# Kernel tuning notes

Hardware: AMD Instinct MI355X
Metric: run time of the kernel (lower is better)

The kernel has to match this reference:

```python
import jax, jax.numpy as jnp
import numpy as np

V, B, NP, NJ = 5, 32, 20, 17
NB = 16
ND = 128
POSE_MIN_DEPTH, POSE_MAX_DEPTH = 2000.0, 8000.0
POSE_SIGMA = 100.0
KS = 11
HIDDEN_ROUGH, HIDDEN = 1024, 1024
BONES = np.array([[0,1],[0,2],[1,3],[2,4],[5,6],[5,7],[7,9],[6,8],[8,10],[5,11],[6,12],[11,12],[11,13],[13,15],[12,14],[14,16]], dtype=np.int32)


def setup_inputs() -> dict:
    key = jax.random.key(0)
    ks = jax.random.split(key, 12)
    wh = jnp.array([1920.0, 1080.0], jnp.float32)
    kpts = jax.random.uniform(ks[0], (V, B, NP, NJ, 2), jnp.float32) * wh
    pose_vis = jnp.ones((V, B, NP), jnp.float32)
    joint_vis = (jax.random.uniform(ks[1], (V, B, NP, NJ)) > 0.15).astype(jnp.float32)
    gt_pose_depths = jax.random.uniform(ks[2], (B, NP), jnp.float32, 2000.0, 8000.0)
    gt_joint_depths = jax.random.uniform(ks[3], (B, NP, NJ), jnp.float32, -100.0, 100.0)
    angles = np.linspace(-0.3, 0.3, V)
    Rs = np.stack([np.array([[np.cos(a), 0.0, np.sin(a)], [0.0, 1.0, 0.0], [-np.sin(a), 0.0, np.cos(a)]], dtype=np.float32) for a in angles])
    cam_R = jnp.broadcast_to(jnp.asarray(Rs)[:, None], (V, B, 3, 3))
    tvec = np.zeros((V, 3), np.float32); tvec[:, 0] = np.linspace(-500.0, 500.0, V)
    cam_T = jnp.broadcast_to(jnp.asarray(tvec)[:, None], (V, B, 3))
    cam_f = jnp.full((V, B, 2), 1400.0, jnp.float32)
    cam_c = jnp.broadcast_to(jnp.array([960.0, 540.0], jnp.float32), (V, B, 2))
    image_wh = jnp.broadcast_to(jnp.array([1920.0, 1080.0], jnp.float32), (V, B, 2))
    num_persons = jax.random.randint(ks[4], (V, B), 10, NP + 1, jnp.int32)
    Wr1 = jax.random.normal(ks[5], (HIDDEN_ROUGH, NJ * 2)) * 0.02
    br1 = jnp.zeros((HIDDEN_ROUGH,), jnp.float32)
    Wr2 = jax.random.normal(ks[6], (NJ, HIDDEN_ROUGH)) * 0.02
    br2 = jnp.zeros((NJ,), jnp.float32)
    Wc1 = jax.random.normal(ks[7], (HIDDEN, NJ + NB, 3)) * 0.02
    bc1 = jnp.zeros((HIDDEN,), jnp.float32)
    Wc2 = jax.random.normal(ks[8], (1, HIDDEN, 3)) * 0.02
    bc2 = jnp.zeros((1,), jnp.float32)
    bones = jnp.asarray(BONES)
    return dict(kpts=kpts, pose_vis=pose_vis, joint_vis=joint_vis, gt_pose_depths=gt_pose_depths, gt_joint_depths=gt_joint_depths, cam_R=cam_R, cam_T=cam_T, cam_f=cam_f, cam_c=cam_c, image_wh=image_wh, num_persons=num_persons, Wr1=Wr1, br1=br1, Wr2=Wr2, br2=br2, Wc1=Wc1, bc1=bc1, Wc2=Wc2, bc2=bc2, bones=bones)


def _bone_len(p, bones):
    # p: [B, Np, Nj, D, 2] -> [B, Np, Nb, D]
    a = p[:, :, bones[:, 0]]
    b = p[:, :, bones[:, 1]]
    return jnp.sqrt(jnp.sum((a - b) ** 2, -1) + 1e-12)


def _conv1d(x, w, b):
    # x [N,C,L], w [O,I,3]
    y = jax.lax.conv_general_dilated(x, w, (1,), 'SAME', dimension_numbers=('NCH', 'OIH', 'NCH'))
    return y + b[None, :, None]


def _forward(kpts, joint_vis, cam_R, cam_T, cam_f, cam_c, image_wh, num_persons, Wr1, br1, Wr2, br2, Wc1, bc1, Wc2, bc2, bones):
    V_, B_, NP_, NJ_, _ = kpts.shape
    labels = jnp.arange(ND, dtype=jnp.float32) / (ND - 1) * (POSE_MAX_DEPTH - POSE_MIN_DEPTH) + POSE_MIN_DEPTH
    kt = kpts[0]  # target-view 2D poses [B,Np,Nj,2]
    # faithful to original indexing quirk: normalize all batches by batch-0 image size
    kn = kt / image_wh[0, 0][None, None, None, :]
    x = kn.reshape(B_ * NP_, NJ_ * 2)
    h = jax.nn.relu(x @ Wr1.T + br1)
    rough = (h @ Wr2.T + br2).reshape(B_, NP_, NJ_) * 1000.0
    rough = jax.lax.stop_gradient(rough)  # .detach() in original
    depths = labels[None, None, None, :] + rough[..., None]  # [B,Np,Nj,D]
    # back-project target 2D poses at every depth hypothesis
    R0, T0, f0, c0 = cam_R[0], cam_T[0], cam_f[0], cam_c[0]
    uvn = (kt - c0[:, None, None, :]) / f0[:, None, None, :]
    xy = uvn[..., None, :] * depths[..., None]
    cam_pts = jnp.concatenate([xy, depths[..., None]], -1)
    p3d = jnp.einsum('bji,bpkdj->bpkdi', R0, cam_pts) + T0[:, None, None, None, :]  # world [B,Np,Nj,D,3]

    scores = scores2 = boundings = boundings2 = None
    for rv in range(1, V_):
        Rr, Tr, fr, cr = cam_R[rv], cam_T[rv], cam_f[rv], cam_c[rv]
        xc = jnp.einsum('bij,bpkdj->bpkdi', Rr, p3d - Tr[:, None, None, None, :])
        p2t = xc[..., :2] / (xc[..., 2:3] + 1e-8) * fr[:, None, None, None, :] + cr[:, None, None, None, :]
        pr = kpts[rv]         # [B,Npr,Nj,2]
        vr = joint_vis[rv]    # [B,Npr,Nj]
        # pairwise dist over (target-person, ref-person) per joint/depth
        d = jnp.sum((p2t[:, :, None] - pr[:, None, :, :, None, :]) ** 2, -1)  # [B,Npt,Npr,Nj,D]
        w = vr[:, None, :, :, None]
        pdist = jnp.sum(d * w, 3) / (jnp.sum(w, 3) + 1e-8)  # [B,Npt,Npr,D]
        valid = jnp.arange(NP_)[None, None, :, None] < num_persons[rv][:, None, None, None]
        pdist = jnp.where(valid, pdist, 1e5)
        mm = jnp.argmin(pdist, 2)  # [B,Npt,D] nearest ref pose
        bidx = jnp.arange(B_)[:, None, None]
        matched = jnp.transpose(pr[bidx, mm], (0, 1, 3, 2, 4))  # [B,Npt,Nj,D,2]
        mvis = jnp.transpose(vr[bidx, mm], (0, 1, 3, 2))        # [B,Npt,Nj,D]
        mdist = jnp.sum((p2t - matched) ** 2, -1)
        score = jnp.exp(-jnp.sqrt(mdist + 1e-12) / POSE_SIGMA)  # panoptic branch
        score_bl = jnp.exp(-jnp.abs(_bone_len(matched, bones) - _bone_len(p2t, bones)) / 5.0)
        wimg = image_wh[rv][:, None, None, None, 0]
        himg = image_wh[rv][:, None, None, None, 1]
        inb = ((p2t[..., 0] >= 0) & (p2t[..., 1] >= 0) & (p2t[..., 0] <= wimg - 1) & (p2t[..., 1] <= himg - 1)).astype(score.dtype)
        bounding = inb * mvis
        bounding2 = jnp.broadcast_to(mvis[:, :, :1, :], score_bl.shape)
        if scores is None:
            scores, scores2 = score * bounding, score_bl * bounding2
            boundings, boundings2 = bounding, bounding2
        else:
            scores = scores + score * bounding
            scores2 = scores2 + score_bl * bounding2
            boundings = boundings + bounding
            boundings2 = boundings2 + bounding2
    psv = (scores / (boundings + 1e-8)).reshape(B_ * NP_, NJ_, ND)
    psv2 = (scores2 / (boundings2 + 1e-8)).reshape(B_ * NP_, NB, ND)
    xin = jnp.concatenate([psv, psv2], 1)  # [BN, Nj+Nb, D]
    hc = jax.nn.relu(_conv1d(xin, Wc1, bc1))
    logits = _conv1d(hc, Wc2, bc2)[:, 0, :]  # [BN, D]
    vol = jax.nn.softmax(logits, -1)
    # soft-argmax restricted to a window around the argmax
    pos = jnp.arange(ND, dtype=vol.dtype)
    idx = jnp.argmax(vol, -1)
    mask = (jnp.abs(pos[None, :] - idx[:, None].astype(vol.dtype)) <= KS // 2).astype(vol.dtype)
    mv = vol * mask
    mv = mv / (jnp.sum(mv, -1, keepdims=True) + 1e-8)
    pred_idx = jnp.sum(mv * pos, -1).reshape(B_, NP_)
    return pred_idx / (ND - 1) * (POSE_MAX_DEPTH - POSE_MIN_DEPTH) + POSE_MIN_DEPTH


def reference(kpts, pose_vis, joint_vis, gt_pose_depths, gt_joint_depths, cam_R, cam_T, cam_f, cam_c, image_wh, num_persons, Wr1, br1, Wr2, br2, Wc1, bc1, Wc2, bc2, bones):
    return _forward(kpts, joint_vis, cam_R, cam_T, cam_f, cam_c, image_wh, num_persons, Wr1, br1, Wr2, br2, Wc1, bc1, Wc2, bc2, bones)
```

## Files before the change

kernel.cpp:

```cpp
#include <hip/hip_runtime.h>
#include <math.h>

#define VV  5
#define BB  32
#define NPP 20
#define NJJ 17
#define NBB 16
#define NDD 128
#define HID 1024
#define KPITCH 128
#define KSTEPS 7
#define PRP 36
#define VRP 20
#define NCH 34
#define A_T_ELEMS (32 * KSTEPS * 64 * 8)
#define EPI_ELEMS (32 * 4 * 64 * 16)

typedef __attribute__((ext_vector_type(8))) short short8;
typedef __attribute__((ext_vector_type(16))) float float16;

static constexpr int BONE_A[NBB] = {0,0,1,2,5,5,7,6,8,5,6,11,11,13,12,14};
static constexpr int BONE_B[NBB] = {1,2,3,4,6,7,9,8,10,11,12,12,13,15,14,16};

__device__ __forceinline__ float warp_red_sum(float v) {
#pragma unroll
  for (int off = 32; off >= 1; off >>= 1) v += __shfl_xor(v, off, 64);
  return v;
}

__global__ __launch_bounds__(256) void prep_kernel(
    const float* __restrict__ Wc1, const float* __restrict__ Wc2,
    const float* __restrict__ bc1,
    unsigned short* __restrict__ A_hi, unsigned short* __restrict__ A_lo,
    float* __restrict__ epi) {
  int gidx = blockIdx.x * 256 + threadIdx.x;
  if (gidx < A_T_ELEMS) {
    int e = gidx & 7;
    int l = (gidx >> 3) & 63;
    int rest = gidx >> 9;
    int ks = rest % 7;
    int ot = rest / 7;
    int o = ot * 32 + (l & 31);
    int kk = ks * 16 + (l >> 5) * 8 + e;
    float x = (kk < 99) ? Wc1[o * 99 + kk] : 0.0f;
    unsigned int u = __float_as_uint(x);
    unsigned short hi = (unsigned short)(u >> 16);
    float xh = __uint_as_float((u >> 16) << 16);
    unsigned short lo = (unsigned short)(__float_as_uint(x - xh) >> 16);
    A_hi[gidx] = hi;
    A_lo[gidx] = lo;
  } else {
    int idx2 = gidx - A_T_ELEMS;
    if (idx2 < EPI_ELEMS) {
      int c = idx2 & 15;
      int l = (idx2 >> 4) & 63;
      int rb = (idx2 >> 10) & 3;
      int ot = idx2 >> 12;
      int base = ot * 32 + 4 * (l >> 5) + 8 * rb;
      epi[idx2] = (c < 12) ? Wc2[base * 3 + c] : bc1[base + (c - 12)];
    }
  }
}

__global__ __launch_bounds__(512, 4) void pose_front_kernel(
    const float* __restrict__ kpts, const float* __restrict__ joint_vis,
    const float* __restrict__ cam_R, const float* __restrict__ cam_T,
    const float* __restrict__ cam_f, const float* __restrict__ cam_c,
    const float* __restrict__ image_wh, const int* __restrict__ num_persons,
    const float* __restrict__ Wr1, const float* __restrict__ br1,
    const float* __restrict__ Wr2, const float* __restrict__ br2,
    float* __restrict__ ws_partial) {
  const int n = blockIdx.x;
  const int b = n / NPP;
  const int p = n % NPP;
  const int tid = threadIdx.x;
  const int wv = tid >> 6, ln = tid & 63;
  const int rvv = tid >> 7;
  const int d   = tid & (NDD - 1);

  __shared__ float sh_x[NJJ * 2];
  __shared__ float sh_h[HID];
  __shared__ float sh_rough[NJJ];
  __shared__ float sh_base[NJJ][3];
  __shared__ __align__(16) float sh_pr[4][NPP][PRP];
  __shared__ __align__(16) float sh_vr[4][NPP][VRP];

  if (tid < NJJ * 2) {
    int j = tid >> 1, c = tid & 1;
    float k = kpts[((size_t)(b * NPP + p)) * NJJ * 2 + j * 2 + c];
    sh_x[tid] = k / image_wh[c];
  }
  __syncthreads();

#pragma unroll
  for (int k = 0; k < 2; ++k) {
    int m = tid + k * 512;
    float acc = br1[m];
#pragma unroll
    for (int c = 0; c < NJJ * 2; ++c) acc = fmaf(Wr1[m * (NJJ * 2) + c], sh_x[c], acc);
    sh_h[m] = fmaxf(acc, 0.0f);
  }
  __syncthreads();

  for (int j = wv; j < NJJ; j += 8) {
    float part = 0.0f;
    for (int m = ln; m < HID; m += 64) part = fmaf(Wr2[j * HID + m], sh_h[m], part);
    part = warp_red_sum(part);
    if (ln == 0) sh_rough[j] = (part + br2[j]) * 1000.0f;
  }
  if (tid < NJJ) {
    int j = tid;
    const float* R0 = cam_R + (size_t)b * 9;
    float c0x = cam_c[b * 2 + 0], c0y = cam_c[b * 2 + 1];
    float f0x = cam_f[b * 2 + 0], f0y = cam_f[b * 2 + 1];
    float kx = kpts[((size_t)(b * NPP + p)) * NJJ * 2 + j * 2 + 0];
    float ky = kpts[((size_t)(b * NPP + p)) * NJJ * 2 + j * 2 + 1];
    float ux = (kx - c0x) / f0x;
    float uy = (ky - c0y) / f0y;
#pragma unroll
    for (int i = 0; i < 3; ++i)
      sh_base[j][i] = R0[0 * 3 + i] * ux + R0[1 * 3 + i] * uy + R0[2 * 3 + i];
  }
#pragma unroll
  for (int rr = 0; rr < 4; ++rr) {
    const float* prg = kpts + ((size_t)(rr + 1) * BB + b) * NPP * NJJ * 2;
    for (int idx = tid; idx < NPP * NJJ * 2; idx += 512)
      sh_pr[rr][idx / 34][idx % 34] = prg[idx];
    const float* vrg = joint_vis + ((size_t)(rr + 1) * BB + b) * NPP * NJJ;
    for (int idx = tid; idx < NPP * NJJ; idx += 512)
      sh_vr[rr][idx / 17][idx % 17] = vrg[idx];
  }
  if (tid < 4 * BB) {
    int rr = tid >> 5, q = tid & 31;
    if (q < NPP) {
      sh_pr[rr][q][34] = 0.0f; sh_pr[rr][q][35] = 0.0f;
      sh_vr[rr][q][17] = 0.0f; sh_vr[rr][q][18] = 0.0f; sh_vr[rr][q][19] = 0.0f;
    }
  }
  __syncthreads();

  {
    const int rv = rvv + 1;
    const int vb = rv * BB + b;
    const float* Rr = cam_R + (size_t)vb * 9;
    const float R00 = Rr[0], R01 = Rr[1], R02 = Rr[2];
    const float R10 = Rr[3], R11 = Rr[4], R12 = Rr[5];
    const float R20 = Rr[6], R21 = Rr[7], R22 = Rr[8];
    const float Trx = cam_T[vb * 3 + 0], Try = cam_T[vb * 3 + 1], Trz = cam_T[vb * 3 + 2];
    const float frx = cam_f[vb * 2 + 0], fry = cam_f[vb * 2 + 1];
    const float crx = cam_c[vb * 2 + 0], cry = cam_c[vb * 2 + 1];
    const float wmax = image_wh[vb * 2 + 0] - 1.0f;
    const float hmax = image_wh[vb * 2 + 1] - 1.0f;
    const int nprv = num_persons[vb];
    const float T0x = cam_T[b * 3 + 0], T0y = cam_T[b * 3 + 1], T0z = cam_T[b * 3 + 2];
    const float lab = ((float)d / 127.0f) * 6000.0f + 2000.0f;

    float px[NJJ], py[NJJ];
#pragma unroll
    for (int j = 0; j < NJJ; ++j) {
      float dep = lab + sh_rough[j];
      float p0 = fmaf(dep, sh_base[j][0], T0x);
      float p1 = fmaf(dep, sh_base[j][1], T0y);
      float p2 = fmaf(dep, sh_base[j][2], T0z);
      float q0 = p0 - Trx, q1 = p1 - Try, q2 = p2 - Trz;
      float xc0 = R00 * q0 + R01 * q1 + R02 * q2;
      float xc1 = R10 * q0 + R11 * q1 + R12 * q2;
      float xc2 = R20 * q0 + R21 * q1 + R22 * q2 + 1e-8f;
      px[j] = xc0 / xc2 * frx + crx;
      py[j] = xc1 / xc2 * fry + cry;
    }

    float best = 3.4e38f;
    int mm = 0;
#pragma unroll 1
    for (int q = 0; q < NPP; ++q) {
      const float4* pr4 = (const float4*)(&sh_pr[rvv][q][0]);
      const float4* vr4 = (const float4*)(&sh_vr[rvv][q][0]);
      float num = 0.0f, den = 0.0f;
#pragma unroll
      for (int g4 = 0; g4 < 4; ++g4) {
        float4 w  = vr4[g4];
        float4 pa = pr4[2 * g4 + 0];
        float4 pb = pr4[2 * g4 + 1];
        { float dx = px[4*g4+0] - pa.x, dy = py[4*g4+0] - pa.y; num = fmaf(w.x, dx*dx + dy*dy, num); den += w.x; }
        { float dx = px[4*g4+1] - pa.z, dy = py[4*g4+1] - pa.w; num = fmaf(w.y, dx*dx + dy*dy, num); den += w.y; }
        { float dx = px[4*g4+2] - pb.x, dy = py[4*g4+2] - pb.y; num = fmaf(w.z, dx*dx + dy*dy, num); den += w.z; }
        { float dx = px[4*g4+3] - pb.z, dy = py[4*g4+3] - pb.w; num = fmaf(w.w, dx*dx + dy*dy, num); den += w.w; }
      }
      {
        float w16 = sh_vr[rvv][q][16];
        float4 pc = pr4[8];
        float dx = px[16] - pc.x, dy = py[16] - pc.y;
        num = fmaf(w16, dx*dx + dy*dy, num); den += w16;
      }
      float pd = num / (den + 1e-8f);
      if (q >= nprv) pd = 100000.0f;
      if (pd < best) { best = pd; mm = q; }
    }

    float* pbase = ws_partial + (((size_t)n * NCH) * 4 + rvv) * 128 + d;
    unsigned int maskB = 0u;
#pragma unroll
    for (int j = 0; j < NJJ; ++j) {
      float mx = sh_pr[rvv][mm][j * 2 + 0];
      float my = sh_pr[rvv][mm][j * 2 + 1];
      float mv = sh_vr[rvv][mm][j];
      float dx = px[j] - mx, dy = py[j] - my;
      float sc = expf(-sqrtf(dx * dx + dy * dy + 1e-12f) / 100.0f);
      float inb = (px[j] >= 0.0f && py[j] >= 0.0f && px[j] <= wmax && py[j] <= hmax) ? 1.0f : 0.0f;
      float bd = inb * mv;
      pbase[j * 512] = sc * bd;
      maskB |= ((unsigned int)(bd != 0.0f)) << j;
    }
    float v0 = sh_vr[rvv][mm][0];
    maskB |= ((unsigned int)(v0 != 0.0f)) << 17;
#pragma unroll
    for (int nb = 0; nb < NBB; ++nb) {
      const int a = BONE_A[nb], c = BONE_B[nb];
      float ax = sh_pr[rvv][mm][a * 2 + 0], ay = sh_pr[rvv][mm][a * 2 + 1];
      float cx = sh_pr[rvv][mm][c * 2 + 0], cy = sh_pr[rvv][mm][c * 2 + 1];
      float dmx = ax - cx, dmy = ay - cy;
      float blm = sqrtf(dmx * dmx + dmy * dmy + 1e-12f);
      float dpx = px[a] - px[c], dpy = py[a] - py[c];
      float blp = sqrtf(dpx * dpx + dpy * dpy + 1e-12f);
      float scb = expf(-fabsf(blm - blp) / 5.0f);
      pbase[(NJJ + nb) * 512] = scb * v0;
    }
    *(unsigned int*)(pbase + 33 * 512) = maskB;
  }
}

__global__ __launch_bounds__(128) void reduce_kernel(
    const float* __restrict__ ws_partial, float* __restrict__ ws_xin) {
  const int n = blockIdx.x;
  const int t = threadIdx.x;
  const float* pb = ws_partial + ((size_t)n * NCH) * 4 * 128;
  float* xo = ws_xin + (size_t)n * (NJJ + NBB) * NDD;

  unsigned int m0 = __float_as_uint(pb[(33 * 4 + 0) * 128 + t]);
  unsigned int m1 = __float_as_uint(pb[(33 * 4 + 1) * 128 + t]);
  unsigned int m2 = __float_as_uint(pb[(33 * 4 + 2) * 128 + t]);
  unsigned int m3 = __float_as_uint(pb[(33 * 4 + 3) * 128 + t]);

#pragma unroll
  for (int i = 0; i < NJJ; ++i) {
    const float* a = pb + (i * 4) * 128 + t;
    float s = ((a[0] + a[128]) + a[256]) + a[384];
    int bj = ((m0 >> i) & 1) + ((m1 >> i) & 1) + ((m2 >> i) & 1) + ((m3 >> i) & 1);
    xo[i * NDD + t] = s / ((float)bj + 1e-8f);
  }
  int b2 = ((m0 >> 17) & 1) + ((m1 >> 17) & 1) + ((m2 >> 17) & 1) + ((m3 >> 17) & 1);
  float den2 = (float)b2 + 1e-8f;
#pragma unroll
  for (int nb = 0; nb < NBB; ++nb) {
    const float* a = pb + ((NJJ + nb) * 4) * 128 + t;
    float s = ((a[0] + a[128]) + a[256]) + a[384];
    xo[(NJJ + nb) * NDD + t] = s / den2;
  }
}

__global__ __launch_bounds__(512, 2) void conv_mfma_kernel(
    const float* __restrict__ ws_xin,
    const unsigned short* __restrict__ A_hi, const unsigned short* __restrict__ A_lo,
    const float* __restrict__ epi,
    const float* __restrict__ bc2, float* __restrict__ out) {
  const int n = blockIdx.x;
  const int tid = threadIdx.x;
  const int w = tid >> 6;
  const int l = tid & 63;
  const int lrow = l & 31;
  const int g = l >> 5;

  __shared__ __align__(16) unsigned short bT_hi[128 * KPITCH];
  __shared__ __align__(16) unsigned short bT_lo[128 * KPITCH];
  __shared__ float plg[3][8][NDD];
  __shared__ float sh_l[NDD];
  __shared__ float sh_e[NDD];
  __shared__ float sh_sc[2];

  for (int i = tid; i < 3 * 8 * NDD; i += 512) ((float*)plg)[i] = 0.0f;

  const float* xn = ws_xin + (size_t)n * (NJJ + NBB) * NDD;
  for (int idx = tid; idx < 64 * 128; idx += 512) {
    const int kp = (idx & 63) << 1;
    const int t  = idx >> 6;
    unsigned int hp = 0, lp = 0;
#pragma unroll
    for (int u = 0; u < 2; ++u) {
      const int kk = kp + u;
      float x = 0.0f;
      if (kk < 99) {
        int i3 = kk / 3;
        int k3 = kk - i3 * 3;
        int tt = t + k3 - 1;
        if (tt >= 0 && tt < 128) x = xn[i3 * NDD + tt];
      }
      unsigned int uu = __float_as_uint(x);
      unsigned int hi = uu >> 16;
      float xh = __uint_as_float(hi << 16);
      unsigned int lo = __float_as_uint(x - xh) >> 16;
      hp |= hi << (16 * u);
      lp |= lo << (16 * u);
    }
    const int e = t * KPITCH + (kp ^ ((t & 15) << 3));
    *(unsigned int*)(bT_hi + e) = hp;
    *(unsigned int*)(bT_lo + e) = lp;
  }
  __syncthreads();

#pragma unroll 1
  for (int otile = 0; otile < 4; ++otile) {
    const int otg = w * 4 + otile;

    short8 Ah[KSTEPS], Al[KSTEPS];
    {
      const short8* ahT = ((const short8*)A_hi) + (size_t)otg * KSTEPS * 64 + l;
      const short8* alT = ((const short8*)A_lo) + (size_t)otg * KSTEPS * 64 + l;
#pragma unroll
      for (int ks = 0; ks < KSTEPS; ++ks) {
        Ah[ks] = ahT[ks * 64];
        Al[ks] = alT[ks * 64];
      }
    }
    float w2f[48];
    float bcf[16];
#pragma unroll
    for (int rb = 0; rb < 4; ++rb) {
      const float4* ep = ((const float4*)epi) + ((size_t)(otg * 4 + rb) * 64 + l) * 4;
      float4 e0 = ep[0], e1 = ep[1], e2 = ep[2], e3 = ep[3];
      w2f[rb * 12 + 0] = e0.x;  w2f[rb * 12 + 1] = e0.y;  w2f[rb * 12 + 2] = e0.z;
      w2f[rb * 12 + 3] = e0.w;  w2f[rb * 12 + 4] = e1.x;  w2f[rb * 12 + 5] = e1.y;
      w2f[rb * 12 + 6] = e1.z;  w2f[rb * 12 + 7] = e1.w;  w2f[rb * 12 + 8] = e2.x;
      w2f[rb * 12 + 9] = e2.y;  w2f[rb * 12 + 10] = e2.z; w2f[rb * 12 + 11] = e2.w;
      bcf[rb * 4 + 0] = e3.x; bcf[rb * 4 + 1] = e3.y;
      bcf[rb * 4 + 2] = e3.z; bcf[rb * 4 + 3] = e3.w;
    }

#pragma unroll 1
    for (int ttile = 0; ttile < 4; ++ttile) {
      const int trow = ttile * 32 + lrow;
      const unsigned short* brh = bT_hi + trow * KPITCH;
      const unsigned short* brl = bT_lo + trow * KPITCH;
      const int sw = (trow & 15) << 3;

      float16 X, Y;
#pragma unroll
      for (int r = 0; r < 16; ++r) { X[r] = 0.0f; Y[r] = 0.0f; }

#pragma unroll
      for (int ks = 0; ks < KSTEPS; ++ks) {
        const int e = (ks * 16 + g * 8) ^ sw;
        short8 bh = *(const short8*)(brh + e);
        X = __builtin_amdgcn_mfma_f32_32x32x16_bf16(Ah[ks], bh, X, 0, 0, 0);
        Y = __builtin_amdgcn_mfma_f32_32x32x16_bf16(Al[ks], bh, Y, 0, 0, 0);
      }
#pragma unroll
      for (int ks = 0; ks < KSTEPS; ++ks) {
        const int e = (ks * 16 + g * 8) ^ sw;
        short8 bl = *(const short8*)(brl + e);
        if (ks & 1) Y = __builtin_amdgcn_mfma_f32_32x32x16_bf16(Ah[ks], bl, Y, 0, 0, 0);
        else        X = __builtin_amdgcn_mfma_f32_32x32x16_bf16(Ah[ks], bl, X, 0, 0, 0);
      }

      float sP = 0.0f, sC = 0.0f, sM = 0.0f;
#pragma unroll
      for (int r = 0; r < 16; ++r) {
        float h = fmaxf((X[r] + Y[r]) + bcf[(r >> 2) * 4 + (r & 3)], 0.0f);
        sP = fmaf(h, w2f[(r >> 2) * 12 + (r & 3) * 3 + 0], sP);
        sC = fmaf(h, w2f[(r >> 2) * 12 + (r & 3) * 3 + 1], sC);
        sM = fmaf(h, w2f[(r >> 2) * 12 + (r & 3) * 3 + 2], sM);
      }
      sP += __shfl_xor(sP, 32, 64);
      sC += __shfl_xor(sC, 32, 64);
      sM += __shfl_xor(sM, 32, 64);
      if (l < 32) {
        plg[0][w][trow] += sP;
        plg[1][w][trow] += sC;
        plg[2][w][trow] += sM;
      }
    }
  }
  __syncthreads();

  if (tid < NDD) {
    int t = tid;
    float lg = bc2[0];
#pragma unroll
    for (int ww = 0; ww < 8; ++ww) lg += plg[1][ww][t];
    if (t > 0) {
#pragma unroll
      for (int ww = 0; ww < 8; ++ww) lg += plg[0][ww][t - 1];
    }
    if (t < NDD - 1) {
#pragma unroll
      for (int ww = 0; ww < 8; ++ww) lg += plg[2][ww][t + 1];
    }
    sh_l[t] = lg;
  }
  __syncthreads();
  if (tid < 64) {
    float v1 = sh_l[tid], v2 = sh_l[tid + 64];
    float mv; int mi;
    if (v2 > v1) { mv = v2; mi = tid + 64; } else { mv = v1; mi = tid; }
#pragma unroll
    for (int off = 32; off >= 1; off >>= 1) {
      float ov = __shfl_xor(mv, off, 64);
      int   oi = __shfl_xor(mi, off, 64);
      if (ov > mv || (ov == mv && oi < mi)) { mv = ov; mi = oi; }
    }
    if (tid == 0) { sh_sc[0] = mv; ((int*)sh_sc)[1] = mi; }
  }
  __syncthreads();
  const float gmax = sh_sc[0];
  const int gidx = ((const int*)sh_sc)[1];
  if (tid < NDD) sh_e[tid] = expf(sh_l[tid] - gmax);
  __syncthreads();
  if (tid < 64) {
    float S = warp_red_sum(sh_e[tid] + sh_e[tid + 64]);
    float a1 = 0.0f, a2 = 0.0f;
#pragma unroll
    for (int k = 0; k < 2; ++k) {
      int t = tid + k * 64;
      float vol = sh_e[t] / S;
      float msk = (fabsf((float)t - (float)gidx) <= 5.0f) ? 1.0f : 0.0f;
      float mvv = vol * msk;
      a1 += mvv;
      a2 += mvv * (float)t;
    }
    a1 = warp_red_sum(a1);
    a2 = warp_red_sum(a2);
    if (tid == 0) {
      float pred = a2 / (a1 + 1e-8f);
      out[n] = pred / 127.0f * 6000.0f + 2000.0f;
    }
  }
}

extern "C" void kernel_launch(void* const* d_in, const int* in_sizes, int n_in,
                              void* d_out, int out_size, void* d_ws, size_t ws_size,
                              hipStream_t stream) {
  (void)in_sizes; (void)n_in; (void)out_size; (void)ws_size;
  const float* kpts        = (const float*)d_in[0];
  const float* joint_vis   = (const float*)d_in[2];
  const float* cam_R       = (const float*)d_in[5];
  const float* cam_T       = (const float*)d_in[6];
  const float* cam_f       = (const float*)d_in[7];
  const float* cam_c       = (const float*)d_in[8];
  const float* image_wh    = (const float*)d_in[9];
  const int*   num_persons = (const int*)d_in[10];
  const float* Wr1 = (const float*)d_in[11];
  const float* br1 = (const float*)d_in[12];
  const float* Wr2 = (const float*)d_in[13];
  const float* br2 = (const float*)d_in[14];
  const float* Wc1 = (const float*)d_in[15];
  const float* bc1 = (const float*)d_in[16];
  const float* Wc2 = (const float*)d_in[17];
  const float* bc2 = (const float*)d_in[18];
  float* out = (float*)d_out;

  unsigned short* A_hi = (unsigned short*)d_ws;
  unsigned short* A_lo = A_hi + A_T_ELEMS;
  float* epi        = (float*)(A_lo + A_T_ELEMS);
  float* ws_xin     = epi + EPI_ELEMS;
  float* ws_partial = ws_xin + (size_t)BB * NPP * (NJJ + NBB) * NDD;

  const int prep_items = A_T_ELEMS + EPI_ELEMS;
  hipLaunchKernelGGL(prep_kernel, dim3((prep_items + 255) / 256), dim3(256), 0, stream,
                     Wc1, Wc2, bc1, A_hi, A_lo, epi);
  hipLaunchKernelGGL(pose_front_kernel, dim3(BB * NPP), dim3(512), 0, stream,
                     kpts, joint_vis, cam_R, cam_T, cam_f, cam_c, image_wh,
                     num_persons, Wr1, br1, Wr2, br2, ws_partial);
  hipLaunchKernelGGL(reduce_kernel, dim3(BB * NPP), dim3(128), 0, stream,
                     ws_partial, ws_xin);
  hipLaunchKernelGGL(conv_mfma_kernel, dim3(BB * NPP), dim3(512), 0, stream,
                     ws_xin, A_hi, A_lo, epi, bc2, out);
}
```

Measured before the change: 181.7 us.

## Split pose front and conv kernels into finer-grained blocks over depth halves

The front kernel is split into a per-person MLP/base kernel and a matching kernel launched with two 256-thread blocks per person, each covering half the depth bins. The conv MFMA kernel likewise runs two 256-thread blocks per person over depth halves and writes partial logits to workspace. A new readout kernel then combines the halves and does the softmax and windowed soft-argmax. This doubles block count to improve occupancy and load balance across CUs. In exchange it adds two extra launches and extra global round-trips for intermediates, and each MFMA block now reloads the A fragments for 8 output tiles per wave instead of 4.

```diff
diff --git a/kernel.cpp b/kernel.cpp
--- a/kernel.cpp
+++ b/kernel.cpp
@@ -13,6 +13,8 @@
 #define PRP 36
 #define VRP 20
 #define NCH 34
+#define RGH_P 20
+#define BASE_P 52
 #define A_T_ELEMS (32 * KSTEPS * 64 * 8)
 #define EPI_ELEMS (32 * 4 * 64 * 16)
 
@@ -62,28 +64,21 @@
   }
 }
 
-__global__ __launch_bounds__(512, 4) void pose_front_kernel(
-    const float* __restrict__ kpts, const float* __restrict__ joint_vis,
-    const float* __restrict__ cam_R, const float* __restrict__ cam_T,
+__global__ __launch_bounds__(256) void pose_pre_kernel(
+    const float* __restrict__ kpts, const float* __restrict__ cam_R,
     const float* __restrict__ cam_f, const float* __restrict__ cam_c,
-    const float* __restrict__ image_wh, const int* __restrict__ num_persons,
+    const float* __restrict__ image_wh,
     const float* __restrict__ Wr1, const float* __restrict__ br1,
     const float* __restrict__ Wr2, const float* __restrict__ br2,
-    float* __restrict__ ws_partial) {
+    float* __restrict__ ws_rough, float* __restrict__ ws_base) {
   const int n = blockIdx.x;
   const int b = n / NPP;
   const int p = n % NPP;
   const int tid = threadIdx.x;
   const int wv = tid >> 6, ln = tid & 63;
-  const int rvv = tid >> 7;
-  const int d   = tid & (NDD - 1);
 
   __shared__ float sh_x[NJJ * 2];
   __shared__ float sh_h[HID];
-  __shared__ float sh_rough[NJJ];
-  __shared__ float sh_base[NJJ][3];
-  __shared__ __align__(16) float sh_pr[4][NPP][PRP];
-  __shared__ __align__(16) float sh_vr[4][NPP][VRP];
 
   if (tid < NJJ * 2) {
     int j = tid >> 1, c = tid & 1;
@@ -93,8 +88,8 @@
   __syncthreads();
 
 #pragma unroll
-  for (int k = 0; k < 2; ++k) {
-    int m = tid + k * 512;
+  for (int k = 0; k < 4; ++k) {
+    int m = tid + k * 256;
     float acc = br1[m];
 #pragma unroll
     for (int c = 0; c < NJJ * 2; ++c) acc = fmaf(Wr1[m * (NJJ * 2) + c], sh_x[c], acc);
@@ -102,12 +97,13 @@
   }
   __syncthreads();
 
-  for (int j = wv; j < NJJ; j += 8) {
+  for (int j = wv; j < NJJ; j += 4) {
     float part = 0.0f;
     for (int m = ln; m < HID; m += 64) part = fmaf(Wr2[j * HID + m], sh_h[m], part);
     part = warp_red_sum(part);
-    if (ln == 0) sh_rough[j] = (part + br2[j]) * 1000.0f;
-  }
+    if (ln == 0) ws_rough[(size_t)n * RGH_P + j] = (part + br2[j]) * 1000.0f;
+  }
+
   if (tid < NJJ) {
     int j = tid;
     const float* R0 = cam_R + (size_t)b * 9;
@@ -119,15 +115,42 @@
     float uy = (ky - c0y) / f0y;
 #pragma unroll
     for (int i = 0; i < 3; ++i)
-      sh_base[j][i] = R0[0 * 3 + i] * ux + R0[1 * 3 + i] * uy + R0[2 * 3 + i];
-  }
+      ws_base[(size_t)n * BASE_P + j * 3 + i] =
+          R0[0 * 3 + i] * ux + R0[1 * 3 + i] * uy + R0[2 * 3 + i];
+  }
+}
+
+__global__ __launch_bounds__(256, 4) void pose_match_kernel(
+    const float* __restrict__ kpts, const float* __restrict__ joint_vis,
+    const float* __restrict__ cam_R, const float* __restrict__ cam_T,
+    const float* __restrict__ cam_f, const float* __restrict__ cam_c,
+    const float* __restrict__ image_wh, const int* __restrict__ num_persons,
+    const float* __restrict__ ws_rough, const float* __restrict__ ws_base,
+    float* __restrict__ ws_partial) {
+  const int bid = blockIdx.x;
+  const int n = bid >> 1;
+  const int bh = bid & 1;
+  const int b = n / NPP;
+  const int tid = threadIdx.x;
+  const int rvv = tid >> 6;
+  const int d = bh * 64 + (tid & 63);
+
+  __shared__ float sh_rough[NJJ];
+  __shared__ float sh_base[NJJ][3];
+  __shared__ __align__(16) float sh_pr[4][NPP][PRP];
+  __shared__ __align__(16) float sh_vr[4][NPP][VRP];
+
+  if (tid < NJJ) sh_rough[tid] = ws_rough[(size_t)n * RGH_P + tid];
+  if (tid >= 64 && tid < 64 + NJJ * 3)
+    ((float*)sh_base)[tid - 64] = ws_base[(size_t)n * BASE_P + (tid - 64)];
+
 #pragma unroll
   for (int rr = 0; rr < 4; ++rr) {
     const float* prg = kpts + ((size_t)(rr + 1) * BB + b) * NPP * NJJ * 2;
-    for (int idx = tid; idx < NPP * NJJ * 2; idx += 512)
+    for (int idx = tid; idx < NPP * NJJ * 2; idx += 256)
       sh_pr[rr][idx / 34][idx % 34] = prg[idx];
     const float* vrg = joint_vis + ((size_t)(rr + 1) * BB + b) * NPP * NJJ;
-    for (int idx = tid; idx < NPP * NJJ; idx += 512)
+    for (int idx = tid; idx < NPP * NJJ; idx += 256)
       sh_vr[rr][idx / 17][idx % 17] = vrg[idx];
   }
   if (tid < 4 * BB) {
@@ -259,31 +282,31 @@
   }
 }
 
-__global__ __launch_bounds__(512, 2) void conv_mfma_kernel(
+__global__ __launch_bounds__(256, 2) void conv_mfma_kernel(
     const float* __restrict__ ws_xin,
     const unsigned short* __restrict__ A_hi, const unsigned short* __restrict__ A_lo,
     const float* __restrict__ epi,
-    const float* __restrict__ bc2, float* __restrict__ out) {
-  const int n = blockIdx.x;
+    float* __restrict__ ws_pcm) {
+  const int bid = blockIdx.x;
+  const int n = bid >> 1;
+  const int bh = bid & 1;
   const int tid = threadIdx.x;
   const int w = tid >> 6;
   const int l = tid & 63;
   const int lrow = l & 31;
   const int g = l >> 5;
 
-  __shared__ __align__(16) unsigned short bT_hi[128 * KPITCH];
-  __shared__ __align__(16) unsigned short bT_lo[128 * KPITCH];
-  __shared__ float plg[3][8][NDD];
-  __shared__ float sh_l[NDD];
-  __shared__ float sh_e[NDD];
-  __shared__ float sh_sc[2];
-
-  for (int i = tid; i < 3 * 8 * NDD; i += 512) ((float*)plg)[i] = 0.0f;
+  __shared__ __align__(16) unsigned short bT_hi[64 * KPITCH];
+  __shared__ __align__(16) unsigned short bT_lo[64 * KPITCH];
+  __shared__ float plg[3][4][64];
+
+  for (int i = tid; i < 3 * 4 * 64; i += 256) ((float*)plg)[i] = 0.0f;
 
   const float* xn = ws_xin + (size_t)n * (NJJ + NBB) * NDD;
-  for (int idx = tid; idx < 64 * 128; idx += 512) {
+  for (int idx = tid; idx < 64 * 64; idx += 256) {
     const int kp = (idx & 63) << 1;
-    const int t  = idx >> 6;
+    const int tl = idx >> 6;
+    const int tg = bh * 64 + tl;
     unsigned int hp = 0, lp = 0;
 #pragma unroll
     for (int u = 0; u < 2; ++u) {
@@ -292,7 +315,7 @@
       if (kk < 99) {
         int i3 = kk / 3;
         int k3 = kk - i3 * 3;
-        int tt = t + k3 - 1;
+        int tt = tg + k3 - 1;
         if (tt >= 0 && tt < 128) x = xn[i3 * NDD + tt];
       }
       unsigned int uu = __float_as_uint(x);
@@ -302,15 +325,15 @@
       hp |= hi << (16 * u);
       lp |= lo << (16 * u);
     }
-    const int e = t * KPITCH + (kp ^ ((t & 15) << 3));
+    const int e = tl * KPITCH + (kp ^ ((tl & 15) << 3));
     *(unsigned int*)(bT_hi + e) = hp;
     *(unsigned int*)(bT_lo + e) = lp;
   }
   __syncthreads();
 
 #pragma unroll 1
-  for (int otile = 0; otile < 4; ++otile) {
-    const int otg = w * 4 + otile;
+  for (int oi = 0; oi < 8; ++oi) {
+    const int otg = w * 8 + oi;
 
     short8 Ah[KSTEPS], Al[KSTEPS];
     {
@@ -337,7 +360,7 @@
     }
 
 #pragma unroll 1
-    for (int ttile = 0; ttile < 4; ++ttile) {
+    for (int ttile = 0; ttile < 2; ++ttile) {
       const int trow = ttile * 32 + lrow;
       const unsigned short* brh = bT_hi + trow * KPITCH;
       const unsigned short* brl = bT_lo + trow * KPITCH;
@@ -350,16 +373,16 @@
 #pragma unroll
       for (int ks = 0; ks < KSTEPS; ++ks) {
         const int e = (ks * 16 + g * 8) ^ sw;
-        short8 bh = *(const short8*)(brh + e);
-        X = __builtin_amdgcn_mfma_f32_32x32x16_bf16(Ah[ks], bh, X, 0, 0, 0);
-        Y = __builtin_amdgcn_mfma_f32_32x32x16_bf16(Al[ks], bh, Y, 0, 0, 0);
+        short8 bh8 = *(const short8*)(brh + e);
+        X = __builtin_amdgcn_mfma_f32_32x32x16_bf16(Ah[ks], bh8, X, 0, 0, 0);
+        Y = __builtin_amdgcn_mfma_f32_32x32x16_bf16(Al[ks], bh8, Y, 0, 0, 0);
       }
 #pragma unroll
       for (int ks = 0; ks < KSTEPS; ++ks) {
         const int e = (ks * 16 + g * 8) ^ sw;
-        short8 bl = *(const short8*)(brl + e);
-        if (ks & 1) Y = __builtin_amdgcn_mfma_f32_32x32x16_bf16(Ah[ks], bl, Y, 0, 0, 0);
-        else        X = __builtin_amdgcn_mfma_f32_32x32x16_bf16(Ah[ks], bl, X, 0, 0, 0);
+        short8 bl8 = *(const short8*)(brl + e);
+        if (ks & 1) Y = __builtin_amdgcn_mfma_f32_32x32x16_bf16(Ah[ks], bl8, Y, 0, 0, 0);
+        else        X = __builtin_amdgcn_mfma_f32_32x32x16_bf16(Ah[ks], bl8, X, 0, 0, 0);
       }
 
       float sP = 0.0f, sC = 0.0f, sM = 0.0f;
@@ -382,54 +405,68 @@
   }
   __syncthreads();
 
-  if (tid < NDD) {
-    int t = tid;
-    float lg = bc2[0];
-#pragma unroll
-    for (int ww = 0; ww < 8; ++ww) lg += plg[1][ww][t];
-    if (t > 0) {
-#pragma unroll
-      for (int ww = 0; ww < 8; ++ww) lg += plg[0][ww][t - 1];
-    }
-    if (t < NDD - 1) {
-#pragma unroll
-      for (int ww = 0; ww < 8; ++ww) lg += plg[2][ww][t + 1];
-    }
-    sh_l[t] = lg;
-  }
-  __syncthreads();
-  if (tid < 64) {
-    float v1 = sh_l[tid], v2 = sh_l[tid + 64];
+  if (tid < 3 * 64) {
+    const int c = tid >> 6, tl = tid & 63;
+    float s = ((plg[c][0][tl] + plg[c][1][tl]) + plg[c][2][tl]) + plg[c][3][tl];
+    ws_pcm[(((size_t)n * 2 + bh) * 3 + c) * 64 + tl] = s;
+  }
+}
+
+__global__ __launch_bounds__(128) void readout_kernel(
+    const float* __restrict__ ws_pcm, const float* __restrict__ bc2,
+    float* __restrict__ out) {
+  const int n = blockIdx.x;
+  const int t = threadIdx.x;
+
+  __shared__ float sh_l[NDD];
+  __shared__ float sh_e[NDD];
+  __shared__ float sh_sc[2];
+
+  const float* pc = ws_pcm + (size_t)n * 2 * 3 * 64;
+  float lg = bc2[0] + pc[((t >> 6) * 3 + 1) * 64 + (t & 63)];
+  if (t > 0) {
+    int tp = t - 1;
+    lg += pc[((tp >> 6) * 3 + 0) * 64 + (tp & 63)];
+  }
+  if (t < NDD - 1) {
+    int tn = t + 1;
+    lg += pc[((tn >> 6) * 3 + 2) * 64 + (tn & 63)];
+  }
+  sh_l[t] = lg;
+  __syncthreads();
+
+  if (t < 64) {
+    float v1 = sh_l[t], v2 = sh_l[t + 64];
     float mv; int mi;
-    if (v2 > v1) { mv = v2; mi = tid + 64; } else { mv = v1; mi = tid; }
+    if (v2 > v1) { mv = v2; mi = t + 64; } else { mv = v1; mi = t; }
 #pragma unroll
     for (int off = 32; off >= 1; off >>= 1) {
       float ov = __shfl_xor(mv, off, 64);
       int   oi = __shfl_xor(mi, off, 64);
       if (ov > mv || (ov == mv && oi < mi)) { mv = ov; mi = oi; }
     }
-    if (tid == 0) { sh_sc[0] = mv; ((int*)sh_sc)[1] = mi; }
+    if (t == 0) { sh_sc[0] = mv; ((int*)sh_sc)[1] = mi; }
   }
   __syncthreads();
   const float gmax = sh_sc[0];
   const int gidx = ((const int*)sh_sc)[1];
-  if (tid < NDD) sh_e[tid] = expf(sh_l[tid] - gmax);
-  __syncthreads();
-  if (tid < 64) {
-    float S = warp_red_sum(sh_e[tid] + sh_e[tid + 64]);
+  sh_e[t] = expf(sh_l[t] - gmax);
+  __syncthreads();
+  if (t < 64) {
+    float S = warp_red_sum(sh_e[t] + sh_e[t + 64]);
     float a1 = 0.0f, a2 = 0.0f;
 #pragma unroll
     for (int k = 0; k < 2; ++k) {
-      int t = tid + k * 64;
-      float vol = sh_e[t] / S;
-      float msk = (fabsf((float)t - (float)gidx) <= 5.0f) ? 1.0f : 0.0f;
+      int tt = t + k * 64;
+      float vol = sh_e[tt] / S;
+      float msk = (fabsf((float)tt - (float)gidx) <= 5.0f) ? 1.0f : 0.0f;
       float mvv = vol * msk;
       a1 += mvv;
-      a2 += mvv * (float)t;
+      a2 += mvv * (float)tt;
     }
     a1 = warp_red_sum(a1);
     a2 = warp_red_sum(a2);
-    if (tid == 0) {
+    if (t == 0) {
       float pred = a2 / (a1 + 1e-8f);
       out[n] = pred / 127.0f * 6000.0f + 2000.0f;
     }
@@ -463,15 +500,23 @@
   float* epi        = (float*)(A_lo + A_T_ELEMS);
   float* ws_xin     = epi + EPI_ELEMS;
   float* ws_partial = ws_xin + (size_t)BB * NPP * (NJJ + NBB) * NDD;
+  float* ws_rough   = ws_partial + (size_t)BB * NPP * NCH * 4 * 128;
+  float* ws_base    = ws_rough + (size_t)BB * NPP * RGH_P;
+  float* ws_pcm     = ws_base + (size_t)BB * NPP * BASE_P;
 
   const int prep_items = A_T_ELEMS + EPI_ELEMS;
   hipLaunchKernelGGL(prep_kernel, dim3((prep_items + 255) / 256), dim3(256), 0, stream,
                      Wc1, Wc2, bc1, A_hi, A_lo, epi);
-  hipLaunchKernelGGL(pose_front_kernel, dim3(BB * NPP), dim3(512), 0, stream,
+  hipLaunchKernelGGL(pose_pre_kernel, dim3(BB * NPP), dim3(256), 0, stream,
+                     kpts, cam_R, cam_f, cam_c, image_wh, Wr1, br1, Wr2, br2,
+                     ws_rough, ws_base);
+  hipLaunchKernelGGL(pose_match_kernel, dim3(BB * NPP * 2), dim3(256), 0, stream,
                      kpts, joint_vis, cam_R, cam_T, cam_f, cam_c, image_wh,
-                     num_persons, Wr1, br1, Wr2, br2, ws_partial);
+                     num_persons, ws_rough, ws_base, ws_partial);
   hipLaunchKernelGGL(reduce_kernel, dim3(BB * NPP), dim3(128), 0, stream,
                      ws_partial, ws_xin);
-  hipLaunchKernelGGL(conv_mfma_kernel, dim3(BB * NPP), dim3(512), 0, stream,
-                     ws_xin, A_hi, A_lo, epi, bc2, out);
-}
+  hipLaunchKernelGGL(conv_mfma_kernel, dim3(BB * NPP * 2), dim3(256), 0, stream,
+                     ws_xin, A_hi, A_lo, epi, ws_pcm);
+  hipLaunchKernelGGL(readout_kernel, dim3(BB * NPP), dim3(128), 0, stream,
+                     ws_pcm, bc2, out);
+}
```

Result: slower. 186.5 us (+2.7%).

## Split pose front into MLP and per-view match kernels, fuse reduction into conv

Applied to the files above, without the earlier changes.

The fused front kernel is split into a 256-thread MLP/base-ray kernel and a 128-thread match kernel launched per (person, view), so each block loads only one view's keypoints and runs with finer-grained blocks. The separate reduce kernel is removed and the cross-view averaging is folded into the conv kernel's input staging, which now reads the four partials and mask words directly. This trades one launch and the xin round trip for an extra launch, a workspace round trip for rough/base values, and redundant partial reads in conv staging (each value is read for three taps).

```diff
diff --git a/kernel.cpp b/kernel.cpp
--- a/kernel.cpp
+++ b/kernel.cpp
@@ -13,6 +13,8 @@
 #define PRP 36
 #define VRP 20
 #define NCH 34
+#define RGH_P 20
+#define BASE_P 52
 #define A_T_ELEMS (32 * KSTEPS * 64 * 8)
 #define EPI_ELEMS (32 * 4 * 64 * 16)
 
@@ -62,28 +64,21 @@
   }
 }
 
-__global__ __launch_bounds__(512, 4) void pose_front_kernel(
-    const float* __restrict__ kpts, const float* __restrict__ joint_vis,
-    const float* __restrict__ cam_R, const float* __restrict__ cam_T,
+__global__ __launch_bounds__(256) void pose_pre_kernel(
+    const float* __restrict__ kpts, const float* __restrict__ cam_R,
     const float* __restrict__ cam_f, const float* __restrict__ cam_c,
-    const float* __restrict__ image_wh, const int* __restrict__ num_persons,
+    const float* __restrict__ image_wh,
     const float* __restrict__ Wr1, const float* __restrict__ br1,
     const float* __restrict__ Wr2, const float* __restrict__ br2,
-    float* __restrict__ ws_partial) {
+    float* __restrict__ ws_rough, float* __restrict__ ws_base) {
   const int n = blockIdx.x;
   const int b = n / NPP;
   const int p = n % NPP;
   const int tid = threadIdx.x;
   const int wv = tid >> 6, ln = tid & 63;
-  const int rvv = tid >> 7;
-  const int d   = tid & (NDD - 1);
 
   __shared__ float sh_x[NJJ * 2];
   __shared__ float sh_h[HID];
-  __shared__ float sh_rough[NJJ];
-  __shared__ float sh_base[NJJ][3];
-  __shared__ __align__(16) float sh_pr[4][NPP][PRP];
-  __shared__ __align__(16) float sh_vr[4][NPP][VRP];
 
   if (tid < NJJ * 2) {
     int j = tid >> 1, c = tid & 1;
@@ -93,8 +88,8 @@
   __syncthreads();
 
 #pragma unroll
-  for (int k = 0; k < 2; ++k) {
-    int m = tid + k * 512;
+  for (int k = 0; k < 4; ++k) {
+    int m = tid + k * 256;
     float acc = br1[m];
 #pragma unroll
     for (int c = 0; c < NJJ * 2; ++c) acc = fmaf(Wr1[m * (NJJ * 2) + c], sh_x[c], acc);
@@ -102,12 +97,13 @@
   }
   __syncthreads();
 
-  for (int j = wv; j < NJJ; j += 8) {
+  for (int j = wv; j < NJJ; j += 4) {
     float part = 0.0f;
     for (int m = ln; m < HID; m += 64) part = fmaf(Wr2[j * HID + m], sh_h[m], part);
     part = warp_red_sum(part);
-    if (ln == 0) sh_rough[j] = (part + br2[j]) * 1000.0f;
-  }
+    if (ln == 0) ws_rough[(size_t)n * RGH_P + j] = (part + br2[j]) * 1000.0f;
+  }
+
   if (tid < NJJ) {
     int j = tid;
     const float* R0 = cam_R + (size_t)b * 9;
@@ -119,22 +115,47 @@
     float uy = (ky - c0y) / f0y;
 #pragma unroll
     for (int i = 0; i < 3; ++i)
-      sh_base[j][i] = R0[0 * 3 + i] * ux + R0[1 * 3 + i] * uy + R0[2 * 3 + i];
-  }
-#pragma unroll
-  for (int rr = 0; rr < 4; ++rr) {
-    const float* prg = kpts + ((size_t)(rr + 1) * BB + b) * NPP * NJJ * 2;
-    for (int idx = tid; idx < NPP * NJJ * 2; idx += 512)
-      sh_pr[rr][idx / 34][idx % 34] = prg[idx];
-    const float* vrg = joint_vis + ((size_t)(rr + 1) * BB + b) * NPP * NJJ;
-    for (int idx = tid; idx < NPP * NJJ; idx += 512)
-      sh_vr[rr][idx / 17][idx % 17] = vrg[idx];
-  }
-  if (tid < 4 * BB) {
-    int rr = tid >> 5, q = tid & 31;
+      ws_base[(size_t)n * BASE_P + j * 3 + i] =
+          R0[0 * 3 + i] * ux + R0[1 * 3 + i] * uy + R0[2 * 3 + i];
+  }
+}
+
+__global__ __launch_bounds__(128, 4) void pose_match_kernel(
+    const float* __restrict__ kpts, const float* __restrict__ joint_vis,
+    const float* __restrict__ cam_R, const float* __restrict__ cam_T,
+    const float* __restrict__ cam_f, const float* __restrict__ cam_c,
+    const float* __restrict__ image_wh, const int* __restrict__ num_persons,
+    const float* __restrict__ ws_rough, const float* __restrict__ ws_base,
+    float* __restrict__ ws_partial) {
+  const int bid = blockIdx.x;
+  const int n = bid >> 2;
+  const int rvv = bid & 3;
+  const int b = n / NPP;
+  const int tid = threadIdx.x;
+  const int d = tid;
+
+  __shared__ float sh_rough[NJJ];
+  __shared__ float sh_base[NJJ][3];
+  __shared__ __align__(16) float sh_pr[NPP][PRP];
+  __shared__ __align__(16) float sh_vr[NPP][VRP];
+
+  if (tid < NJJ) sh_rough[tid] = ws_rough[(size_t)n * RGH_P + tid];
+  if (tid >= 64 && tid < 64 + NJJ * 3)
+    ((float*)sh_base)[tid - 64] = ws_base[(size_t)n * BASE_P + (tid - 64)];
+
+  {
+    const float* prg = kpts + ((size_t)(rvv + 1) * BB + b) * NPP * NJJ * 2;
+    for (int idx = tid; idx < NPP * NJJ * 2; idx += 128)
+      sh_pr[idx / 34][idx % 34] = prg[idx];
+    const float* vrg = joint_vis + ((size_t)(rvv + 1) * BB + b) * NPP * NJJ;
+    for (int idx = tid; idx < NPP * NJJ; idx += 128)
+      sh_vr[idx / 17][idx % 17] = vrg[idx];
+  }
+  if (tid < BB) {
+    int q = tid;
     if (q < NPP) {
-      sh_pr[rr][q][34] = 0.0f; sh_pr[rr][q][35] = 0.0f;
-      sh_vr[rr][q][17] = 0.0f; sh_vr[rr][q][18] = 0.0f; sh_vr[rr][q][19] = 0.0f;
+      sh_pr[q][34] = 0.0f; sh_pr[q][35] = 0.0f;
+      sh_vr[q][17] = 0.0f; sh_vr[q][18] = 0.0f; sh_vr[q][19] = 0.0f;
     }
   }
   __syncthreads();
@@ -174,8 +195,8 @@
     int mm = 0;
 #pragma unroll 1
     for (int q = 0; q < NPP; ++q) {
-      const float4* pr4 = (const float4*)(&sh_pr[rvv][q][0]);
-      const float4* vr4 = (const float4*)(&sh_vr[rvv][q][0]);
+      const float4* pr4 = (const float4*)(&sh_pr[q][0]);
+      const float4* vr4 = (const float4*)(&sh_vr[q][0]);
       float num = 0.0f, den = 0.0f;
 #pragma unroll
       for (int g4 = 0; g4 < 4; ++g4) {
@@ -188,7 +209,7 @@
         { float dx = px[4*g4+3] - pb.z, dy = py[4*g4+3] - pb.w; num = fmaf(w.w, dx*dx + dy*dy, num); den += w.w; }
       }
       {
-        float w16 = sh_vr[rvv][q][16];
+        float w16 = sh_vr[q][16];
         float4 pc = pr4[8];
         float dx = px[16] - pc.x, dy = py[16] - pc.y;
         num = fmaf(w16, dx*dx + dy*dy, num); den += w16;
@@ -202,9 +223,9 @@
     unsigned int maskB = 0u;
 #pragma unroll
     for (int j = 0; j < NJJ; ++j) {
-      float mx = sh_pr[rvv][mm][j * 2 + 0];
-      float my = sh_pr[rvv][mm][j * 2 + 1];
-      float mv = sh_vr[rvv][mm][j];
+      float mx = sh_pr[mm][j * 2 + 0];
+      float my = sh_pr[mm][j * 2 + 1];
+      float mv = sh_vr[mm][j];
       float dx = px[j] - mx, dy = py[j] - my;
       float sc = expf(-sqrtf(dx * dx + dy * dy + 1e-12f) / 100.0f);
       float inb = (px[j] >= 0.0f && py[j] >= 0.0f && px[j] <= wmax && py[j] <= hmax) ? 1.0f : 0.0f;
@@ -212,13 +233,13 @@
       pbase[j * 512] = sc * bd;
       maskB |= ((unsigned int)(bd != 0.0f)) << j;
     }
-    float v0 = sh_vr[rvv][mm][0];
+    float v0 = sh_vr[mm][0];
     maskB |= ((unsigned int)(v0 != 0.0f)) << 17;
 #pragma unroll
     for (int nb = 0; nb < NBB; ++nb) {
       const int a = BONE_A[nb], c = BONE_B[nb];
-      float ax = sh_pr[rvv][mm][a * 2 + 0], ay = sh_pr[rvv][mm][a * 2 + 1];
-      float cx = sh_pr[rvv][mm][c * 2 + 0], cy = sh_pr[rvv][mm][c * 2 + 1];
+      float ax = sh_pr[mm][a * 2 + 0], ay = sh_pr[mm][a * 2 + 1];
+      float cx = sh_pr[mm][c * 2 + 0], cy = sh_pr[mm][c * 2 + 1];
       float dmx = ax - cx, dmy = ay - cy;
       float blm = sqrtf(dmx * dmx + dmy * dmy + 1e-12f);
       float dpx = px[a] - px[c], dpy = py[a] - py[c];
@@ -230,37 +251,8 @@
   }
 }
 
-__global__ __launch_bounds__(128) void reduce_kernel(
-    const float* __restrict__ ws_partial, float* __restrict__ ws_xin) {
-  const int n = blockIdx.x;
-  const int t = threadIdx.x;
-  const float* pb = ws_partial + ((size_t)n * NCH) * 4 * 128;
-  float* xo = ws_xin + (size_t)n * (NJJ + NBB) * NDD;
-
-  unsigned int m0 = __float_as_uint(pb[(33 * 4 + 0) * 128 + t]);
-  unsigned int m1 = __float_as_uint(pb[(33 * 4 + 1) * 128 + t]);
-  unsigned int m2 = __float_as_uint(pb[(33 * 4 + 2) * 128 + t]);
-  unsigned int m3 = __float_as_uint(pb[(33 * 4 + 3) * 128 + t]);
-
-#pragma unroll
-  for (int i = 0; i < NJJ; ++i) {
-    const float* a = pb + (i * 4) * 128 + t;
-    float s = ((a[0] + a[128]) + a[256]) + a[384];
-    int bj = ((m0 >> i) & 1) + ((m1 >> i) & 1) + ((m2 >> i) & 1) + ((m3 >> i) & 1);
-    xo[i * NDD + t] = s / ((float)bj + 1e-8f);
-  }
-  int b2 = ((m0 >> 17) & 1) + ((m1 >> 17) & 1) + ((m2 >> 17) & 1) + ((m3 >> 17) & 1);
-  float den2 = (float)b2 + 1e-8f;
-#pragma unroll
-  for (int nb = 0; nb < NBB; ++nb) {
-    const float* a = pb + ((NJJ + nb) * 4) * 128 + t;
-    float s = ((a[0] + a[128]) + a[256]) + a[384];
-    xo[(NJJ + nb) * NDD + t] = s / den2;
-  }
-}
-
 __global__ __launch_bounds__(512, 2) void conv_mfma_kernel(
-    const float* __restrict__ ws_xin,
+    const float* __restrict__ ws_partial,
     const unsigned short* __restrict__ A_hi, const unsigned short* __restrict__ A_lo,
     const float* __restrict__ epi,
     const float* __restrict__ bc2, float* __restrict__ out) {
@@ -280,7 +272,7 @@
 
   for (int i = tid; i < 3 * 8 * NDD; i += 512) ((float*)plg)[i] = 0.0f;
 
-  const float* xn = ws_xin + (size_t)n * (NJJ + NBB) * NDD;
+  const float* pb = ws_partial + ((size_t)n * NCH) * 4 * 128;
   for (int idx = tid; idx < 64 * 128; idx += 512) {
     const int kp = (idx & 63) << 1;
     const int t  = idx >> 6;
@@ -293,7 +285,17 @@
         int i3 = kk / 3;
         int k3 = kk - i3 * 3;
         int tt = t + k3 - 1;
-        if (tt >= 0 && tt < 128) x = xn[i3 * NDD + tt];
+        if (tt >= 0 && tt < 128) {
+          const float* a = pb + ((size_t)i3 * 4) * 128 + tt;
+          float s = ((a[0] + a[128]) + a[256]) + a[384];
+          unsigned int m0 = __float_as_uint(pb[(33 * 4 + 0) * 128 + tt]);
+          unsigned int m1 = __float_as_uint(pb[(33 * 4 + 1) * 128 + tt]);
+          unsigned int m2 = __float_as_uint(pb[(33 * 4 + 2) * 128 + tt]);
+          unsigned int m3 = __float_as_uint(pb[(33 * 4 + 3) * 128 + tt]);
+          const int bit = (i3 < NJJ) ? i3 : 17;
+          int cnt = ((m0 >> bit) & 1) + ((m1 >> bit) & 1) + ((m2 >> bit) & 1) + ((m3 >> bit) & 1);
+          x = s / ((float)cnt + 1e-8f);
+        }
       }
       unsigned int uu = __float_as_uint(x);
       unsigned int hi = uu >> 16;
@@ -350,16 +352,16 @@
 #pragma unroll
       for (int ks = 0; ks < KSTEPS; ++ks) {
         const int e = (ks * 16 + g * 8) ^ sw;
-        short8 bh = *(const short8*)(brh + e);
-        X = __builtin_amdgcn_mfma_f32_32x32x16_bf16(Ah[ks], bh, X, 0, 0, 0);
-        Y = __builtin_amdgcn_mfma_f32_32x32x16_bf16(Al[ks], bh, Y, 0, 0, 0);
+        short8 bh8 = *(const short8*)(brh + e);
+        X = __builtin_amdgcn_mfma_f32_32x32x16_bf16(Ah[ks], bh8, X, 0, 0, 0);
+        Y = __builtin_amdgcn_mfma_f32_32x32x16_bf16(Al[ks], bh8, Y, 0, 0, 0);
       }
 #pragma unroll
       for (int ks = 0; ks < KSTEPS; ++ks) {
         const int e = (ks * 16 + g * 8) ^ sw;
-        short8 bl = *(const short8*)(brl + e);
-        if (ks & 1) Y = __builtin_amdgcn_mfma_f32_32x32x16_bf16(Ah[ks], bl, Y, 0, 0, 0);
-        else        X = __builtin_amdgcn_mfma_f32_32x32x16_bf16(Ah[ks], bl, X, 0, 0, 0);
+        short8 bl8 = *(const short8*)(brl + e);
+        if (ks & 1) Y = __builtin_amdgcn_mfma_f32_32x32x16_bf16(Ah[ks], bl8, Y, 0, 0, 0);
+        else        X = __builtin_amdgcn_mfma_f32_32x32x16_bf16(Ah[ks], bl8, X, 0, 0, 0);
       }
 
       float sP = 0.0f, sC = 0.0f, sM = 0.0f;
@@ -461,17 +463,19 @@
   unsigned short* A_hi = (unsigned short*)d_ws;
   unsigned short* A_lo = A_hi + A_T_ELEMS;
   float* epi        = (float*)(A_lo + A_T_ELEMS);
-  float* ws_xin     = epi + EPI_ELEMS;
-  float* ws_partial = ws_xin + (size_t)BB * NPP * (NJJ + NBB) * NDD;
+  float* ws_partial = epi + EPI_ELEMS;
+  float* ws_rough   = ws_partial + (size_t)BB * NPP * NCH * 4 * 128;
+  float* ws_base    = ws_rough + (size_t)BB * NPP * RGH_P;
 
   const int prep_items = A_T_ELEMS + EPI_ELEMS;
   hipLaunchKernelGGL(prep_kernel, dim3((prep_items + 255) / 256), dim3(256), 0, stream,
                      Wc1, Wc2, bc1, A_hi, A_lo, epi);
-  hipLaunchKernelGGL(pose_front_kernel, dim3(BB * NPP), dim3(512), 0, stream,
+  hipLaunchKernelGGL(pose_pre_kernel, dim3(BB * NPP), dim3(256), 0, stream,
+                     kpts, cam_R, cam_f, cam_c, image_wh, Wr1, br1, Wr2, br2,
+                     ws_rough, ws_base);
+  hipLaunchKernelGGL(pose_match_kernel, dim3(BB * NPP * 4), dim3(128), 0, stream,
                      kpts, joint_vis, cam_R, cam_T, cam_f, cam_c, image_wh,
-                     num_persons, Wr1, br1, Wr2, br2, ws_partial);
-  hipLaunchKernelGGL(reduce_kernel, dim3(BB * NPP), dim3(128), 0, stream,
-                     ws_partial, ws_xin);
+                     num_persons, ws_rough, ws_base, ws_partial);
   hipLaunchKernelGGL(conv_mfma_kernel, dim3(BB * NPP), dim3(512), 0, stream,
-                     ws_xin, A_hi, A_lo, epi, bc2, out);
-}
+                     ws_partial, A_hi, A_lo, epi, bc2, out);
+}
```

New measurement: 214.3 us. 17.9% more time.
